# Performance work log

Measured on AMD Instinct MI355X. Metric: run time of the kernel, lower is better.

## Reference

```python
import jax, jax.numpy as jnp
import numpy as np
import math

D_IN = 4096
D_OUT = 4096
RANK = 8
SCALE = 16.0 / 8.0  # alpha / rank


def fwht(x):
    """Fast Walsh-Hadamard transform over last dim (power of two), orthonormal."""
    d = x.shape[-1]
    orig_shape = x.shape
    h = 1
    while h < d:
        y = x.reshape(x.shape[:-1] + (d // (2 * h), 2, h))
        a = y[..., 0, :]
        b = y[..., 1, :]
        x = jnp.stack([a + b, a - b], axis=-2).reshape(orig_shape)
        h <<= 1
    return x / math.sqrt(d)


def srht_right_multiply(x, signs, perm):
    # x @ P  (sign flip -> column permutation -> FWHT)
    return fwht((x * signs)[..., perm])


def srht_right_multiply_T(x, signs, inv_perm):
    # x @ P^T (FWHT -> inverse permutation -> sign flip)
    return fwht(x)[..., inv_perm] * signs


def setup_inputs() -> dict:
    key = jax.random.key(0)
    ks = jax.random.split(key, 10)
    x = jax.random.normal(ks[0], (4, 2048, D_IN), dtype=jnp.float32)
    W = jax.random.normal(ks[1], (D_OUT, D_IN), dtype=jnp.float32) * 0.02
    b = jax.random.normal(ks[2], (D_OUT,), dtype=jnp.float32) * 0.02
    # kaiming-uniform-ish init for A; random B (real module zero-inits B, but
    # random B exercises the full adapter path for correctness checking)
    bound = 1.0 / math.sqrt(D_IN)
    A = jax.random.uniform(ks[3], (RANK, D_IN), minval=-bound, maxval=bound, dtype=jnp.float32)
    B = jax.random.normal(ks[4], (D_OUT, RANK), dtype=jnp.float32) * 0.02
    in_signs = (jax.random.randint(ks[5], (D_IN,), 0, 2) * 2 - 1).astype(jnp.float32)
    out_signs = (jax.random.randint(ks[6], (D_OUT,), 0, 2) * 2 - 1).astype(jnp.float32)
    in_perm = jax.random.permutation(ks[7], D_IN).astype(jnp.int32)
    in_inv_perm = jnp.argsort(in_perm).astype(jnp.int32)
    out_perm = jax.random.permutation(ks[8], D_OUT).astype(jnp.int32)
    out_inv_perm = jnp.argsort(out_perm).astype(jnp.int32)
    return {
        "x": x, "W": W, "b": b, "A": A, "B": B,
        "in_signs": in_signs, "out_signs": out_signs,
        "in_perm": in_perm, "in_inv_perm": in_inv_perm,
        "out_perm": out_perm, "out_inv_perm": out_inv_perm,
    }


def reference(x, W, b, A, B, in_signs, out_signs, in_perm, in_inv_perm, out_perm, out_inv_perm):
    # base linear
    residual = jnp.einsum('bsi,oi->bso', x, W) + b
    # adapter path: x @ P_in^T @ A^T @ B^T @ P_out, scaled
    adapter_in = srht_right_multiply_T(x, in_signs, in_inv_perm)  # [b,s,in]
    down = jnp.einsum('bsi,ri->bsr', adapter_in, A)               # [b,s,rank]
    up = jnp.einsum('bsr,or->bso', down, B)                       # [b,s,out]
    up = srht_right_multiply(up, out_signs, out_perm)
    return residual + SCALE * up
```

## Files before the change

### kernel.cpp

```cpp
#include <hip/hip_runtime.h>
#include <stdint.h>
#include <stddef.h>

#define DDIM 4096
#define MROWS 8192
#define RANK 8

typedef __attribute__((ext_vector_type(8))) short bf16x8;
typedef __attribute__((ext_vector_type(16))) float f32x16;
typedef __attribute__((ext_vector_type(8))) unsigned short u16x8;

__device__ __forceinline__ unsigned short f2bf(float f) {
  union { float f; unsigned int u; } c; c.f = f;
  unsigned int u = c.u + 0x7fffu + ((c.u >> 16) & 1u);
  return (unsigned short)(u >> 16);
}

__global__ void convert_x_kernel(const float4* __restrict__ x, u16x8* __restrict__ out) {
  int idx = blockIdx.x * 256 + threadIdx.x;
  float4 v0 = x[2 * idx];
  float4 v1 = x[2 * idx + 1];
  u16x8 o;
  o[0] = f2bf(v0.x); o[1] = f2bf(v0.y); o[2] = f2bf(v0.z); o[3] = f2bf(v0.w);
  o[4] = f2bf(v1.x); o[5] = f2bf(v1.y); o[6] = f2bf(v1.z); o[7] = f2bf(v1.w);
  out[idx] = o;
}

__global__ __launch_bounds__(1024) void srht_fold_kernel(
    const float* __restrict__ A, const float* __restrict__ Bm,
    const float* __restrict__ in_signs, const float* __restrict__ out_signs,
    const int* __restrict__ in_perm, const int* __restrict__ out_perm,
    float* __restrict__ A2, float* __restrict__ B2t) {
  __shared__ float buf[DDIM];
  const int tid = threadIdx.x;
  const int b = blockIdx.x;
  if (b < RANK) {
    const int r = b;
    for (int j = tid; j < DDIM; j += 1024) {
      int p = in_perm[j];
      buf[j] = in_signs[p] * A[r * DDIM + p];
    }
  } else {
    const int r = b - RANK;
    for (int j = tid; j < DDIM; j += 1024) {
      int p = out_perm[j];
      buf[j] = out_signs[p] * Bm[p * RANK + r];
    }
  }
  __syncthreads();
  for (int h = 1; h < DDIM; h <<= 1) {
    for (int p = tid; p < DDIM / 2; p += 1024) {
      int j = p & (h - 1);
      int i0 = ((p - j) << 1) + j;
      int i1 = i0 + h;
      float a = buf[i0], c = buf[i1];
      buf[i0] = a + c;
      buf[i1] = a - c;
    }
    __syncthreads();
  }
  const float scale = (b < RANK) ? (1.0f / 64.0f) : (2.0f / 64.0f);
  float* dst = (b < RANK) ? (A2 + b * DDIM) : (B2t + (b - RANK) * DDIM);
  for (int j = tid; j < DDIM; j += 1024) dst[j] = buf[j] * scale;
}

__global__ void weff_kernel(const float4* __restrict__ W, const float* __restrict__ A2,
                            const float* __restrict__ B2t, u16x8* __restrict__ Weff) {
  int idx = blockIdx.x * 256 + threadIdx.x;
  int o = idx >> 9;
  int c8 = idx & 511;
  float4 w0 = W[2 * idx];
  float4 w1 = W[2 * idx + 1];
#pragma unroll
  for (int r = 0; r < RANK; ++r) {
    float s = B2t[r * DDIM + o];
    const float4* av = (const float4*)(A2 + r * DDIM) + 2 * c8;
    float4 a0 = av[0], a1 = av[1];
    w0.x += s * a0.x; w0.y += s * a0.y; w0.z += s * a0.z; w0.w += s * a0.w;
    w1.x += s * a1.x; w1.y += s * a1.y; w1.z += s * a1.z; w1.w += s * a1.w;
  }
  u16x8 u;
  u[0] = f2bf(w0.x); u[1] = f2bf(w0.y); u[2] = f2bf(w0.z); u[3] = f2bf(w0.w);
  u[4] = f2bf(w1.x); u[5] = f2bf(w1.y); u[6] = f2bf(w1.z); u[7] = f2bf(w1.w);
  Weff[idx] = u;
}

__device__ __forceinline__ void async_copy16(const unsigned short* g, unsigned short* l) {
  __builtin_amdgcn_global_load_lds(
      (const __attribute__((address_space(1))) unsigned int*)g,
      (__attribute__((address_space(3))) unsigned int*)l, 16, 0, 0);
}

__global__ __launch_bounds__(256, 2) void gemm_bt_kernel(
    const unsigned short* __restrict__ Ab,
    const unsigned short* __restrict__ Bb,
    const float* __restrict__ bias,
    float* __restrict__ C) {
  constexpr int K = 4096, N = 4096;
  __shared__ unsigned short As[256 * 64];
  __shared__ unsigned short Bs[128 * 64];

  const int tid = threadIdx.x;
  const int pid = blockIdx.x;

  const int GRID_N = 32;
  const int grpsz = 8 * GRID_N;
  const int group = pid / grpsz;
  const int lpid = pid % grpsz;
  const int m_blk = group * 8 + (lpid & 7);
  const int n_blk = lpid >> 3;
  const int mBase = m_blk * 256;
  const int nBase = n_blk * 128;

  const int sr = tid >> 3;
  const int swz_s = (sr & 7) ^ ((sr >> 3) & 3);
  const int sc = (tid & 7) ^ swz_s;
  const unsigned short* ga[8];
  const unsigned short* gb[4];
#pragma unroll
  for (int j = 0; j < 8; ++j)
    ga[j] = Ab + (size_t)(mBase + j * 32 + sr) * K + sc * 8;
#pragma unroll
  for (int j = 0; j < 4; ++j)
    gb[j] = Bb + (size_t)(nBase + j * 32 + sr) * K + sc * 8;
  unsigned short* lA = As + tid * 8;
  unsigned short* lB = Bs + tid * 8;

  const int lane = tid & 63;
  const int wid = tid >> 6;
  const int wm = wid >> 1;
  const int wn = wid & 1;
  const int lm = lane & 31;
  const int half = lane >> 5;
  const int swz_f = (lm & 7) ^ ((lm >> 3) & 3);

  int aoff[4][4], boff[2][4];
#pragma unroll
  for (int mt = 0; mt < 4; ++mt) {
    int r = wm * 128 + mt * 32 + lm;
#pragma unroll
    for (int ks = 0; ks < 4; ++ks) {
      int c = ks * 2 + half;
      aoff[mt][ks] = r * 64 + ((c ^ swz_f) * 8);
    }
  }
#pragma unroll
  for (int nt = 0; nt < 2; ++nt) {
    int r = wn * 64 + nt * 32 + lm;
#pragma unroll
    for (int ks = 0; ks < 4; ++ks) {
      int c = ks * 2 + half;
      boff[nt][ks] = r * 64 + ((c ^ swz_f) * 8);
    }
  }

  f32x16 acc[4][2];
#pragma unroll
  for (int mt = 0; mt < 4; ++mt)
#pragma unroll
    for (int nt = 0; nt < 2; ++nt)
#pragma unroll
      for (int i = 0; i < 16; ++i) acc[mt][nt][i] = 0.f;

  for (int kt = 0; kt < K / 64; ++kt) {
#pragma unroll
    for (int j = 0; j < 8; ++j) async_copy16(ga[j], lA + j * 2048);
#pragma unroll
    for (int j = 0; j < 4; ++j) async_copy16(gb[j], lB + j * 2048);
#pragma unroll
    for (int j = 0; j < 8; ++j) ga[j] += 64;
#pragma unroll
    for (int j = 0; j < 4; ++j) gb[j] += 64;
    __syncthreads();
#pragma unroll
    for (int ks = 0; ks < 4; ++ks) {
      bf16x8 af[4], bfr[2];
#pragma unroll
      for (int mt = 0; mt < 4; ++mt) af[mt] = *(const bf16x8*)(As + aoff[mt][ks]);
#pragma unroll
      for (int nt = 0; nt < 2; ++nt) bfr[nt] = *(const bf16x8*)(Bs + boff[nt][ks]);
#pragma unroll
      for (int mt = 0; mt < 4; ++mt)
#pragma unroll
        for (int nt = 0; nt < 2; ++nt)
          acc[mt][nt] = __builtin_amdgcn_mfma_f32_32x32x16_bf16(af[mt], bfr[nt],
                                                                acc[mt][nt], 0, 0, 0);
    }
    __syncthreads();
  }

#pragma unroll
  for (int nt = 0; nt < 2; ++nt) {
    const int col = nBase + wn * 64 + nt * 32 + lm;
    const float bc = bias[col];
#pragma unroll
    for (int mt = 0; mt < 4; ++mt) {
      const int row0 = mBase + wm * 128 + mt * 32 + 4 * half;
      float* cp = C + (size_t)row0 * N + col;
#pragma unroll
      for (int reg = 0; reg < 16; ++reg) {
        int row = (reg & 3) + 8 * (reg >> 2);
        cp[(size_t)row * N] = acc[mt][nt][reg] + bc;
      }
    }
  }
}

extern "C" void kernel_launch(void* const* d_in, const int* in_sizes, int n_in,
                              void* d_out, int out_size, void* d_ws, size_t ws_size,
                              hipStream_t stream) {
  const float* x        = (const float*)d_in[0];
  const float* W        = (const float*)d_in[1];
  const float* b        = (const float*)d_in[2];
  const float* A        = (const float*)d_in[3];
  const float* Bm       = (const float*)d_in[4];
  const float* in_signs = (const float*)d_in[5];
  const float* out_signs= (const float*)d_in[6];
  const int*   in_perm  = (const int*)d_in[7];
  const int*   out_perm = (const int*)d_in[9];
  float* out = (float*)d_out;

  char* ws = (char*)d_ws;
  unsigned short* x_bf = (unsigned short*)ws;
  unsigned short* weff = (unsigned short*)(ws + (size_t)67108864);
  float* A2  = (float*)(ws + (size_t)67108864 + (size_t)33554432);
  float* B2t = A2 + RANK * DDIM;

  convert_x_kernel<<<16384, 256, 0, stream>>>((const float4*)x, (u16x8*)x_bf);
  srht_fold_kernel<<<16, 1024, 0, stream>>>(A, Bm, in_signs, out_signs, in_perm, out_perm,
                                            A2, B2t);
  weff_kernel<<<8192, 256, 0, stream>>>((const float4*)W, A2, B2t, (u16x8*)weff);
  gemm_bt_kernel<<<1024, 256, 0, stream>>>(x_bf, weff, b, out);
}
```

Before: 582.0 us.

## Rewrite GEMM as 256x256 double-buffered pipeline with interleaved loads and MFMA

The bf16 GEMM moves to 256x256 tiles with 512 threads (8 waves), double-buffered LDS and a hand-scheduled ping-pong loop. Global-to-LDS async loads for the next K tile are interleaved with LDS fragment reads and MFMA clusters, using explicit vmcnt/lgkmcnt waits, barriers and setprio. A new XCD-aware block swizzle maps blocks to tiles. The aim is to hide memory latency and raise arithmetic intensity. In exchange it uses 128KB of LDS, which may limit occupancy, and adds many barriers.

```diff
diff --git a/kernel.cpp b/kernel.cpp
--- a/kernel.cpp
+++ b/kernel.cpp
@@ -91,45 +91,52 @@
       (__attribute__((address_space(3))) unsigned int*)l, 16, 0, 0);
 }
 
-__global__ __launch_bounds__(256, 2) void gemm_bt_kernel(
+#define BARX() __builtin_amdgcn_s_barrier()
+#define LGKM0() asm volatile("s_waitcnt lgkmcnt(0)" ::: "memory")
+#define VMCNT(n) asm volatile("s_waitcnt vmcnt(" #n ")" ::: "memory")
+
+__global__ __launch_bounds__(512, 2) void gemm_bt_kernel(
     const unsigned short* __restrict__ Ab,
     const unsigned short* __restrict__ Bb,
     const float* __restrict__ bias,
     float* __restrict__ C) {
   constexpr int K = 4096, N = 4096;
-  __shared__ unsigned short As[256 * 64];
-  __shared__ unsigned short Bs[128 * 64];
+  __shared__ unsigned short As[2][256 * 64];
+  __shared__ unsigned short Bs[2][256 * 64];
 
   const int tid = threadIdx.x;
   const int pid = blockIdx.x;
-
-  const int GRID_N = 32;
-  const int grpsz = 8 * GRID_N;
-  const int group = pid / grpsz;
-  const int lpid = pid % grpsz;
-  const int m_blk = group * 8 + (lpid & 7);
-  const int n_blk = lpid >> 3;
-  const int mBase = m_blk * 256;
-  const int nBase = n_blk * 128;
+  const int swzp = (pid & 7) * 64 + (pid >> 3);
+  const int gg = swzp >> 7;
+  const int ll = swzp & 127;
+  const int mBase = (gg * 8 + (ll & 7)) * 256;
+  const int nBase = (ll >> 3) * 256;
 
   const int sr = tid >> 3;
   const int swz_s = (sr & 7) ^ ((sr >> 3) & 3);
   const int sc = (tid & 7) ^ swz_s;
-  const unsigned short* ga[8];
-  const unsigned short* gb[4];
-#pragma unroll
-  for (int j = 0; j < 8; ++j)
-    ga[j] = Ab + (size_t)(mBase + j * 32 + sr) * K + sc * 8;
-#pragma unroll
-  for (int j = 0; j < 4; ++j)
-    gb[j] = Bb + (size_t)(nBase + j * 32 + sr) * K + sc * 8;
-  unsigned short* lA = As + tid * 8;
-  unsigned short* lB = Bs + tid * 8;
+  const size_t aOff = (size_t)(mBase + sr) * K + sc * 8;
+  const size_t bOff = (size_t)(nBase + sr) * K + sc * 8;
+
+#define STAGE_A(buf, unit, tt)                                                        \
+  do {                                                                                \
+    async_copy16(Ab + aOff + (size_t)((unit) * 128) * K + (size_t)(tt) * 64,          \
+                 &As[buf][((unit) * 128) * 64 + tid * 8]);                            \
+    async_copy16(Ab + aOff + (size_t)((unit) * 128 + 64) * K + (size_t)(tt) * 64,     \
+                 &As[buf][((unit) * 128 + 64) * 64 + tid * 8]);                       \
+  } while (0)
+#define STAGE_B(buf, unit, tt)                                                        \
+  do {                                                                                \
+    async_copy16(Bb + bOff + (size_t)((unit) * 128) * K + (size_t)(tt) * 64,          \
+                 &Bs[buf][((unit) * 128) * 64 + tid * 8]);                            \
+    async_copy16(Bb + bOff + (size_t)((unit) * 128 + 64) * K + (size_t)(tt) * 64,     \
+                 &Bs[buf][((unit) * 128 + 64) * 64 + tid * 8]);                       \
+  } while (0)
 
   const int lane = tid & 63;
   const int wid = tid >> 6;
-  const int wm = wid >> 1;
-  const int wn = wid & 1;
+  const int wm = wid >> 2;
+  const int wn = wid & 3;
   const int lm = lane & 31;
   const int half = lane >> 5;
   const int swz_f = (lm & 7) ^ ((lm >> 3) & 3);
@@ -162,31 +169,112 @@
 #pragma unroll
       for (int i = 0; i < 16; ++i) acc[mt][nt][i] = 0.f;
 
-  for (int kt = 0; kt < K / 64; ++kt) {
-#pragma unroll
-    for (int j = 0; j < 8; ++j) async_copy16(ga[j], lA + j * 2048);
-#pragma unroll
-    for (int j = 0; j < 4; ++j) async_copy16(gb[j], lB + j * 2048);
-#pragma unroll
-    for (int j = 0; j < 8; ++j) ga[j] += 64;
-#pragma unroll
-    for (int j = 0; j < 4; ++j) gb[j] += 64;
-    __syncthreads();
-#pragma unroll
-    for (int ks = 0; ks < 4; ++ks) {
-      bf16x8 af[4], bfr[2];
-#pragma unroll
-      for (int mt = 0; mt < 4; ++mt) af[mt] = *(const bf16x8*)(As + aoff[mt][ks]);
-#pragma unroll
-      for (int nt = 0; nt < 2; ++nt) bfr[nt] = *(const bf16x8*)(Bs + boff[nt][ks]);
-#pragma unroll
-      for (int mt = 0; mt < 4; ++mt)
-#pragma unroll
-        for (int nt = 0; nt < 2; ++nt)
-          acc[mt][nt] = __builtin_amdgcn_mfma_f32_32x32x16_bf16(af[mt], bfr[nt],
-                                                                acc[mt][nt], 0, 0, 0);
-    }
-    __syncthreads();
+  bf16x8 afr[2][4];
+  bf16x8 bfr[2][4];
+
+#define READ_AF(buf, mh)                                                        \
+  do {                                                                          \
+    _Pragma("unroll") for (int qq = 0; qq < 2; ++qq)                            \
+    _Pragma("unroll") for (int kk = 0; kk < 4; ++kk)                            \
+        afr[qq][kk] = *(const bf16x8*)(&As[buf][aoff[(mh) * 2 + qq][kk]]);      \
+  } while (0)
+#define READ_BF(buf, nh)                                                        \
+  do {                                                                          \
+    _Pragma("unroll") for (int kk = 0; kk < 4; ++kk)                            \
+        bfr[nh][kk] = *(const bf16x8*)(&Bs[buf][boff[nh][kk]]);                 \
+  } while (0)
+#define MFMA8(mh, nh)                                                           \
+  do {                                                                          \
+    __builtin_amdgcn_s_setprio(1);                                              \
+    _Pragma("unroll") for (int kk = 0; kk < 4; ++kk)                            \
+    _Pragma("unroll") for (int qq = 0; qq < 2; ++qq)                            \
+        acc[(mh) * 2 + qq][nh] = __builtin_amdgcn_mfma_f32_32x32x16_bf16(       \
+            afr[qq][kk], bfr[nh][kk], acc[(mh) * 2 + qq][nh], 0, 0, 0);         \
+    __builtin_amdgcn_s_setprio(0);                                              \
+  } while (0)
+
+  STAGE_A(0, 0, 0); STAGE_A(0, 1, 0); STAGE_B(0, 0, 0); STAGE_B(0, 1, 0);
+  STAGE_B(1, 0, 1); STAGE_B(1, 1, 1);
+  VMCNT(4);
+  BARX();
+
+#pragma clang loop unroll(disable)
+  for (int I = 0; I < 31; ++I) {
+    const int t = 2 * I;
+    READ_AF(0, 0); READ_BF(0, 0);
+    STAGE_A(1, 0, t + 1);
+    BARX(); LGKM0();
+    MFMA8(0, 0);
+    BARX();
+    READ_BF(0, 1);
+    STAGE_A(1, 1, t + 1);
+    BARX(); LGKM0();
+    MFMA8(0, 1);
+    BARX();
+    READ_AF(0, 1);
+    STAGE_B(0, 0, t + 2);
+    BARX(); LGKM0();
+    MFMA8(1, 0);
+    BARX();
+    STAGE_B(0, 1, t + 2);
+    BARX();
+    MFMA8(1, 1);
+    VMCNT(4);
+    BARX();
+    READ_AF(1, 0); READ_BF(1, 0);
+    STAGE_A(0, 0, t + 2);
+    BARX(); LGKM0();
+    MFMA8(0, 0);
+    BARX();
+    READ_BF(1, 1);
+    STAGE_A(0, 1, t + 2);
+    BARX(); LGKM0();
+    MFMA8(0, 1);
+    BARX();
+    READ_AF(1, 1);
+    STAGE_B(1, 0, t + 3);
+    BARX(); LGKM0();
+    MFMA8(1, 0);
+    BARX();
+    STAGE_B(1, 1, t + 3);
+    BARX();
+    MFMA8(1, 1);
+    VMCNT(4);
+    BARX();
+  }
+
+  {
+    READ_AF(0, 0); READ_BF(0, 0);
+    STAGE_A(1, 0, 63);
+    BARX(); LGKM0();
+    MFMA8(0, 0);
+    BARX();
+    READ_BF(0, 1);
+    STAGE_A(1, 1, 63);
+    BARX(); LGKM0();
+    MFMA8(0, 1);
+    BARX();
+    READ_AF(0, 1);
+    BARX(); LGKM0();
+    MFMA8(1, 0);
+    BARX();
+    BARX();
+    MFMA8(1, 1);
+    VMCNT(0);
+    BARX();
+    READ_AF(1, 0); READ_BF(1, 0);
+    BARX(); LGKM0();
+    MFMA8(0, 0);
+    BARX();
+    READ_BF(1, 1);
+    BARX(); LGKM0();
+    MFMA8(0, 1);
+    BARX();
+    READ_AF(1, 1);
+    BARX(); LGKM0();
+    MFMA8(1, 0);
+    BARX();
+    MFMA8(1, 1);
   }
 
 #pragma unroll
@@ -230,5 +318,5 @@
   srht_fold_kernel<<<16, 1024, 0, stream>>>(A, Bm, in_signs, out_signs, in_perm, out_perm,
                                             A2, B2t);
   weff_kernel<<<8192, 256, 0, stream>>>((const float4*)W, A2, B2t, (u16x8*)weff);
-  gemm_bt_kernel<<<1024, 256, 0, stream>>>(x_bf, weff, b, out);
-}
+  gemm_bt_kernel<<<512, 512, 0, stream>>>(x_bf, weff, b, out);
+}
```

New measurement: 549.3 us. -5.6%, faster.
